# Kernel optimization log

Hardware: AMD Instinct MI355X
Metric: run time of the kernel (lower is better)

The kernel has to match this reference:

```python
import jax, jax.numpy as jnp
import numpy as np

B, S, V, E, Hd, O = 64, 512, 50000, 512, 1024, 10


def setup_inputs() -> dict:
    key = jax.random.key(0)
    ks = jax.random.split(key, 12)
    inp = {
        "inputs": jax.random.randint(ks[0], (B, S), 0, V),
        "weights": jax.random.normal(ks[1], (V, E), dtype=jnp.float32),
        "W_xr": jax.random.normal(ks[2], (E, Hd), dtype=jnp.float32) / np.sqrt(E),
        "W_hr": jax.random.normal(ks[3], (Hd, Hd), dtype=jnp.float32) / np.sqrt(Hd),
        "b_r": jnp.zeros((Hd,), dtype=jnp.float32),
        "W_xz": jax.random.normal(ks[4], (E, Hd), dtype=jnp.float32) / np.sqrt(E),
        "W_hz": jax.random.normal(ks[5], (Hd, Hd), dtype=jnp.float32) / np.sqrt(Hd),
        "b_z": jnp.ones((Hd,), dtype=jnp.float32),
        "W_xc": jax.random.normal(ks[6], (E, Hd), dtype=jnp.float32) / np.sqrt(E),
        "W_hc": jax.random.normal(ks[7], (Hd, Hd), dtype=jnp.float32) / np.sqrt(Hd),
        "b_c": jnp.zeros((Hd,), dtype=jnp.float32),
        "W_hq": jax.random.normal(ks[8], (Hd, O), dtype=jnp.float32) / np.sqrt(Hd),
        "b_q": jnp.zeros((O,), dtype=jnp.float32),
    }
    return inp


def reference(inputs, weights, W_xr, W_hr, b_r, W_xz, W_hz, b_z,
              W_xc, W_hc, b_c, W_hq, b_q):
    # embed: [B, S, E] -> time-major [S, B, E]
    xs = jnp.swapaxes(weights[inputs], 0, 1)

    def step(H, X):
        r = jax.nn.sigmoid(X @ W_xr + H @ W_hr + b_r)
        z = jax.nn.sigmoid(X @ W_xz + H @ W_hz + b_z)
        h = jnp.tanh(X @ W_xc + (H * r) @ W_hc + b_c)
        H_new = z * H + (1.0 - z) * h
        return H_new, None

    H0 = jnp.zeros((inputs.shape[0], W_hr.shape[0]), dtype=weights.dtype)
    H, _ = jax.lax.scan(step, H0, xs)
    return jax.nn.softmax(H @ W_hq + b_q, axis=1)
```

## Files before the change

kernel.cpp:

```cpp
#include <hip/hip_runtime.h>
#include <stdint.h>

#define S_LEN 512
#define B_SZ  64
#define E_DIM 512
#define HD    1024
#define NGATE 3072
#define O_DIM 10

typedef __attribute__((ext_vector_type(4))) float f32x4;
typedef __attribute__((ext_vector_type(8))) short bf16x8;

__device__ __forceinline__ float bf2f(unsigned short u) {
  union { unsigned int i; float f; } c; c.i = ((unsigned int)u) << 16; return c.f;
}
__device__ __forceinline__ unsigned short f2bf(float f) {
  union { float f; unsigned int i; } c; c.f = f;
  unsigned int u = c.i;
  return (unsigned short)((u + 0x7fffu + ((u >> 16) & 1u)) >> 16);
}
__device__ __forceinline__ float sigmoid_fast(float x) { return 1.0f / (1.0f + __expf(-x)); }
__device__ __forceinline__ float tanh_fast(float x) {
  float a = fabsf(x);
  float e = __expf(2.0f * a);
  return copysignf(1.0f - 2.0f / (e + 1.0f), x);
}
__device__ __forceinline__ f32x4 mfma16(bf16x8 a, bf16x8 b, f32x4 c) {
  return __builtin_amdgcn_mfma_f32_16x16x32_bf16(a, b, c, 0, 0, 0);
}
__device__ __forceinline__ unsigned long long ld_u64_agent(const unsigned long long* p) {
  return __hip_atomic_load(p, __ATOMIC_RELAXED, __HIP_MEMORY_SCOPE_AGENT);
}
__device__ __forceinline__ unsigned int ld_u32_agent(const unsigned int* p) {
  return __hip_atomic_load(p, __ATOMIC_RELAXED, __HIP_MEMORY_SCOPE_AGENT);
}
__device__ __forceinline__ void st_u32_agent(unsigned int* p, unsigned int v) {
  __hip_atomic_store(p, v, __ATOMIC_RELAXED, __HIP_MEMORY_SCOPE_AGENT);
}

#define SLOT_STRIDE 64
#define OFF_HB2   0
#define OFF_RH2   262144
#define OFF_HF    393216
#define OFF_SLOTS 655360
#define OFF_WR    1704960
#define OFF_WZ    3802112
#define OFF_WC    5899264
#define OFF_WX    7996416
#define OFF_XP    11142144

__global__ void convert_kernel(const float* __restrict__ Whr, const float* __restrict__ Whz,
                               const float* __restrict__ Whc,
                               const float* __restrict__ Wxr, const float* __restrict__ Wxz,
                               const float* __restrict__ Wxc,
                               unsigned short* __restrict__ Wr_swz, unsigned short* __restrict__ Wz_swz,
                               unsigned short* __restrict__ Wc_swz, unsigned short* __restrict__ Wx_swz) {
  long idx = (long)blockIdx.x * blockDim.x + threadIdx.x;
  const long NH = (long)HD * HD;
  if (idx < 3 * NH) {
    int m = (int)(idx >> 20);
    int t = (int)(idx & (NH - 1));
    int k = t >> 10, j = t & 1023;
    const float* src = (m == 0) ? Whr : (m == 1) ? Whz : Whc;
    unsigned short* dst = (m == 0) ? Wr_swz : (m == 1) ? Wz_swz : Wc_swz;
    int jt = j >> 4, n = j & 15, kt = k >> 5, q = (k >> 3) & 3, i = k & 7;
    dst[((long)(jt * 32 + kt) * 64 + (q * 16 + n)) * 8 + i] = f2bf(src[(long)k * HD + j]);
  } else {
    long t = idx - 3 * NH;
    if (t < (long)E_DIM * NGATE) {
      int e  = (int)(t / NGATE);
      int jg = (int)(t - (long)e * NGATE);
      int jt = jg >> 4, n = jg & 15, kt = e >> 5, q = (e >> 3) & 3, i = e & 7;
      int gate = jg >> 10, jj = jg & 1023;
      const float* src = (gate == 0) ? Wxr : (gate == 1) ? Wxz : Wxc;
      Wx_swz[((long)(jt * 16 + kt) * 64 + (q * 16 + n)) * 8 + i] = f2bf(src[(long)e * HD + jj]);
    }
  }
}

__launch_bounds__(256, 2)
__global__ void embed_kernel(const int* __restrict__ tokens,
                             const float* __restrict__ Emb,
                             const unsigned short* __restrict__ Wx_swz,
                             const float* __restrict__ b_r, const float* __restrict__ b_z,
                             const float* __restrict__ b_c,
                             unsigned short* __restrict__ Xp) {
  __shared__ unsigned short xl[B_SZ * E_DIM];
  const int s = blockIdx.y;
  const int slab = blockIdx.x;
  const int tid = threadIdx.x;
  for (int it = 0; it < 32; ++it) {
    int task = tid + 256 * it;
    int row = task >> 7;
    int f = task & 127;
    int tok = tokens[row * S_LEN + s];
    float4 v = *(const float4*)(Emb + (long)tok * E_DIM + f * 4);
    int sw = (f >> 1) ^ (row & 7);
    unsigned short* p = xl + row * E_DIM + sw * 8 + (f & 1) * 4;
    p[0] = f2bf(v.x); p[1] = f2bf(v.y); p[2] = f2bf(v.z); p[3] = f2bf(v.w);
  }
  __syncthreads();
  const int lane = tid & 63, wave = tid >> 6;
  const int n = lane & 15, q = lane >> 4;
  const int jt_glob = slab * 4 + wave;
  f32x4 acc[4];
  #pragma unroll
  for (int bt = 0; bt < 4; ++bt) { acc[bt][0]=0.f; acc[bt][1]=0.f; acc[bt][2]=0.f; acc[bt][3]=0.f; }
  for (int kt = 0; kt < 16; ++kt) {
    bf16x8 bfrag = *(const bf16x8*)(Wx_swz + ((long)(jt_glob * 16 + kt) * 64 + lane) * 8);
    #pragma unroll
    for (int bt = 0; bt < 4; ++bt) {
      int row = bt * 16 + n;
      int chunk = (kt * 4 + q) ^ (row & 7);
      bf16x8 afrag = *(const bf16x8*)(xl + row * E_DIM + chunk * 8);
      acc[bt] = mfma16(afrag, bfrag, acc[bt]);
    }
  }
  const int jglob = jt_glob * 16 + n;
  const int gate = jglob >> 10, jj = jglob & 1023;
  const float bias = (gate == 0 ? b_r : gate == 1 ? b_z : b_c)[jj];
  #pragma unroll
  for (int bt = 0; bt < 4; ++bt) {
    unsigned int lo = (unsigned)f2bf(acc[bt][0] + bias) | ((unsigned)f2bf(acc[bt][1] + bias) << 16);
    unsigned int hi = (unsigned)f2bf(acc[bt][2] + bias) | ((unsigned)f2bf(acc[bt][3] + bias) << 16);
    uint2 pk; pk.x = lo; pk.y = hi;
    *(uint2*)(Xp + (((long)s * 4 + bt) * NGATE + jglob) * 16 + q * 4) = pk;
  }
}

__launch_bounds__(256, 1)
__global__ void gru_kernel(const unsigned short* __restrict__ Xp,
                           const unsigned short* __restrict__ Wr_swz,
                           const unsigned short* __restrict__ Wz_swz,
                           const unsigned short* __restrict__ Wc_swz,
                           unsigned short* __restrict__ Hb2,
                           float* __restrict__ Hf,
                           unsigned short* __restrict__ rh2,
                           unsigned int* __restrict__ slots) {
  __shared__ float red[4][6][256];
  __shared__ float zbuf[16 * 32];
  __shared__ float hmaster[16 * 32];

  const int tid = threadIdx.x;
  const int lane = tid & 63, w = tid >> 6;
  const int n = lane & 15, q = lane >> 4;
  const int blk = blockIdx.x;
  const int g  = blk & 3;
  const int bh = blk >> 2;

  const int rr = lane >> 4;
  const int m  = lane & 15;
  const int prow = 4 * w + rr;
  const int pc = 2 * m;
  const int t0 = pc >> 4;
  const int n0 = pc & 15;

  bf16x8 wr_reg[2][8], wz_reg[2][8], wc_reg[2][8];
  #pragma unroll
  for (int jt = 0; jt < 2; ++jt)
    #pragma unroll
    for (int t = 0; t < 8; ++t) {
      long o = ((long)((2 * bh + jt) * 32 + w * 8 + t)) * 512 + lane * 8;
      wr_reg[jt][t] = *(const bf16x8*)(Wr_swz + o);
      wz_reg[jt][t] = *(const bf16x8*)(Wz_swz + o);
      wc_reg[jt][t] = *(const bf16x8*)(Wc_swz + o);
    }
  for (int i = tid; i < 512; i += 256) hmaster[i] = 0.f;
  __syncthreads();

  unsigned int* gslots = slots + g * 128 * SLOT_STRIDE;
  unsigned int* myflag = gslots + (bh * 4 + w) * SLOT_STRIDE;
  const unsigned int* pollp =
      gslots + ((w * 8 + (lane >> 2)) * 4 + (lane & 3)) * SLOT_STRIDE;

  const long xp_step = (long)4 * NGATE * 16;
  const unsigned short* xr_p = Xp + ((long)g * NGATE + bh * 32 + pc) * 16 + prow;
  const unsigned short* xc_p = Xp + ((long)g * NGATE + 2 * HD + bh * 32 + pc) * 16 + prow;
  const unsigned short* xz_p = Xp + ((long)g * NGATE + HD + bh * 32 + (w & 1) * 16 + n) * 16 + q * 4;

  unsigned short xr0 = xr_p[0],  xr1 = xr_p[16];
  unsigned short xc0 = xc_p[0],  xc1 = xc_p[16];
  uint2 xz; xz.x = 0; xz.y = 0;
  if (w >= 2) xz = *(const uint2*)xz_p;

  const long my32 = (long)(g * 32 + bh) * 256 + (long)prow * 16 + m;
  const long ld64 = (long)n * 8 + q * 2;
  const long grp64 = (long)g * 4096;

  unsigned int* rh_u32 = (unsigned int*)rh2;
  unsigned int* hb_u32 = (unsigned int*)Hb2;

  unsigned long long a0[8], a1[8];
  #pragma unroll
  for (int t = 0; t < 8; ++t) { a0[t] = 0ull; a1[t] = 0ull; }

  int cur = 0;
  unsigned int seq = 1;

  for (int s = 0; s < S_LEN; ++s) {
    f32x4 aR0, aR1;
    aR0[0]=0.f;aR0[1]=0.f;aR0[2]=0.f;aR0[3]=0.f; aR1 = aR0;
    #pragma unroll
    for (int t = 0; t < 8; ++t) {
      union { unsigned long long u[2]; bf16x8 v; } af;
      af.u[0] = a0[t]; af.u[1] = a1[t];
      aR0 = mfma16(af.v, wr_reg[0][t], aR0);
      aR1 = mfma16(af.v, wr_reg[1][t], aR1);
    }
    *(f32x4*)&red[w][0][lane * 4] = aR0;
    *(f32x4*)&red[w][1][lane * 4] = aR1;
    __syncthreads();
    {
      float v0 = 0.f, v1 = 0.f;
      #pragma unroll
      for (int k = 0; k < 4; ++k) {
        v0 += red[k][t0][(w * 16 + n0) * 4 + rr];
        v1 += red[k][t0][(w * 16 + n0 + 1) * 4 + rr];
      }
      float r0 = sigmoid_fast(v0 + bf2f(xr0)) * hmaster[prow * 32 + pc];
      float r1 = sigmoid_fast(v1 + bf2f(xr1)) * hmaster[prow * 32 + pc + 1];
      unsigned int pay = (unsigned)f2bf(r0) | ((unsigned)f2bf(r1) << 16);
      st_u32_agent(rh_u32 + my32, pay);
      asm volatile("s_waitcnt vmcnt(0)" ::: "memory");
      if (lane == 0) st_u32_agent(myflag, seq);
    }
    f32x4 aZ0, aZ1;
    aZ0[0]=0.f;aZ0[1]=0.f;aZ0[2]=0.f;aZ0[3]=0.f; aZ1 = aZ0;
    #pragma unroll
    for (int t = 0; t < 8; ++t) {
      union { unsigned long long u[2]; bf16x8 v; } af;
      af.u[0] = a0[t]; af.u[1] = a1[t];
      aZ0 = mfma16(af.v, wz_reg[0][t], aZ0);
      aZ1 = mfma16(af.v, wz_reg[1][t], aZ1);
    }
    *(f32x4*)&red[w][2][lane * 4] = aZ0;
    *(f32x4*)&red[w][3][lane * 4] = aZ1;
    if (lane < 32) { while (ld_u32_agent(pollp) < seq) {} }
    asm volatile("" ::: "memory");
    unsigned long long rA[8], rB[8];
    #pragma unroll
    for (int t = 0; t < 8; ++t) {
      const unsigned long long* p =
          (const unsigned long long*)rh2 + grp64 + (long)(w * 8 + t) * 128 + ld64;
      rA[t] = ld_u64_agent(p);
      rB[t] = ld_u64_agent(p + 1);
    }
    __syncthreads();
    if (w >= 2) {
      const int tz = w - 2;
      f32x4 accz = *(const f32x4*)&red[0][2 + tz][lane * 4];
      #pragma unroll
      for (int k = 1; k < 4; ++k) { f32x4 p = *(const f32x4*)&red[k][2 + tz][lane * 4]; accz += p; }
      #pragma unroll
      for (int r_ = 0; r_ < 4; ++r_) {
        float xpv = bf2f((unsigned short)(((r_ < 2) ? xz.x : xz.y) >> ((r_ & 1) * 16)));
        zbuf[(q * 4 + r_) * 32 + tz * 16 + n] = sigmoid_fast(accz[r_] + xpv);
      }
    }
    f32x4 cA, cB;
    cA[0]=0.f;cA[1]=0.f;cA[2]=0.f;cA[3]=0.f; cB = cA;
    #pragma unroll
    for (int t = 0; t < 8; ++t) {
      union { unsigned long long u[2]; bf16x8 v; } af;
      af.u[0] = rA[t]; af.u[1] = rB[t];
      cA = mfma16(af.v, wc_reg[0][t], cA);
      cB = mfma16(af.v, wc_reg[1][t], cB);
    }
    *(f32x4*)&red[w][4][lane * 4] = cA;
    *(f32x4*)&red[w][5][lane * 4] = cB;
    __syncthreads();
    {
      float v0 = 0.f, v1 = 0.f;
      #pragma unroll
      for (int k = 0; k < 4; ++k) {
        v0 += red[k][4 + t0][(w * 16 + n0) * 4 + rr];
        v1 += red[k][4 + t0][(w * 16 + n0 + 1) * 4 + rr];
      }
      float cv0 = tanh_fast(v0 + bf2f(xc0));
      float cv1 = tanh_fast(v1 + bf2f(xc1));
      float z0 = zbuf[prow * 32 + pc],     z1 = zbuf[prow * 32 + pc + 1];
      float h0 = hmaster[prow * 32 + pc],  h1 = hmaster[prow * 32 + pc + 1];
      float hn0 = z0 * h0 + (1.0f - z0) * cv0;
      float hn1 = z1 * h1 + (1.0f - z1) * cv1;
      hmaster[prow * 32 + pc]     = hn0;
      hmaster[prow * 32 + pc + 1] = hn1;
      if (s == S_LEN - 1) {
        Hf[(long)(g * 16 + prow) * HD + bh * 32 + pc]     = hn0;
        Hf[(long)(g * 16 + prow) * HD + bh * 32 + pc + 1] = hn1;
      }
      unsigned int pay = (unsigned)f2bf(hn0) | ((unsigned)f2bf(hn1) << 16);
      st_u32_agent(hb_u32 + (long)(cur ^ 1) * 32768 + my32, pay);
      asm volatile("s_waitcnt vmcnt(0)" ::: "memory");
      if (lane == 0) st_u32_agent(myflag, seq + 1);
    }
    if (s < S_LEN - 1) {
      const unsigned short* xr_s = xr_p + (long)(s + 1) * xp_step;
      const unsigned short* xc_s = xc_p + (long)(s + 1) * xp_step;
      unsigned short xr0n = xr_s[0], xr1n = xr_s[16];
      unsigned short xc0n = xc_s[0], xc1n = xc_s[16];
      uint2 xzn; xzn.x = 0; xzn.y = 0;
      if (w >= 2) xzn = *(const uint2*)(xz_p + (long)(s + 1) * xp_step);
      if (lane < 32) { while (ld_u32_agent(pollp) < seq + 1) {} }
      asm volatile("" ::: "memory");
      const unsigned long long* hb =
          (const unsigned long long*)Hb2 + (long)(cur ^ 1) * 16384 + grp64;
      #pragma unroll
      for (int t = 0; t < 8; ++t) {
        const unsigned long long* p = hb + (long)(w * 8 + t) * 128 + ld64;
        a0[t] = ld_u64_agent(p);
        a1[t] = ld_u64_agent(p + 1);
      }
      xr0 = xr0n; xr1 = xr1n; xc0 = xc0n; xc1 = xc1n; xz = xzn;
    }
    seq += 2;
    cur ^= 1;
  }
}

__global__ void logits_kernel(const float* __restrict__ Hf, const float* __restrict__ Whq,
                              const float* __restrict__ bq, float* __restrict__ out) {
  const int b = blockIdx.x;
  const int lane = threadIdx.x;
  float acc[O_DIM];
  #pragma unroll
  for (int o = 0; o < O_DIM; ++o) acc[o] = 0.f;
  for (int k = lane; k < HD; k += 64) {
    float h = Hf[(long)b * HD + k];
    #pragma unroll
    for (int o = 0; o < O_DIM; ++o) acc[o] += h * Whq[(long)k * O_DIM + o];
  }
  #pragma unroll
  for (int o = 0; o < O_DIM; ++o) {
    #pragma unroll
    for (int off = 32; off > 0; off >>= 1) acc[o] += __shfl_down(acc[o], off, 64);
  }
  if (lane == 0) {
    float lg[O_DIM], m = -1e30f, sum = 0.f;
    #pragma unroll
    for (int o = 0; o < O_DIM; ++o) { lg[o] = acc[o] + bq[o]; m = fmaxf(m, lg[o]); }
    #pragma unroll
    for (int o = 0; o < O_DIM; ++o) { lg[o] = __expf(lg[o] - m); sum += lg[o]; }
    float inv = 1.0f / sum;
    #pragma unroll
    for (int o = 0; o < O_DIM; ++o) out[(long)b * O_DIM + o] = lg[o] * inv;
  }
}

extern "C" void kernel_launch(void* const* d_in, const int* in_sizes, int n_in,
                              void* d_out, int out_size, void* d_ws, size_t ws_size,
                              hipStream_t stream) {
  const int*   tokens = (const int*)d_in[0];
  const float* Emb = (const float*)d_in[1];
  const float* Wxr = (const float*)d_in[2];
  const float* Whr = (const float*)d_in[3];
  const float* br  = (const float*)d_in[4];
  const float* Wxz = (const float*)d_in[5];
  const float* Whz = (const float*)d_in[6];
  const float* bz  = (const float*)d_in[7];
  const float* Wxc = (const float*)d_in[8];
  const float* Whc = (const float*)d_in[9];
  const float* bc  = (const float*)d_in[10];
  const float* Whq = (const float*)d_in[11];
  const float* bq  = (const float*)d_in[12];

  char* ws = (char*)d_ws;
  unsigned short* Hb2    = (unsigned short*)(ws + OFF_HB2);
  unsigned short* rh2    = (unsigned short*)(ws + OFF_RH2);
  float*          Hf     = (float*)(ws + OFF_HF);
  unsigned int*   slots  = (unsigned int*)(ws + OFF_SLOTS);
  unsigned short* Wr_swz = (unsigned short*)(ws + OFF_WR);
  unsigned short* Wz_swz = (unsigned short*)(ws + OFF_WZ);
  unsigned short* Wc_swz = (unsigned short*)(ws + OFF_WC);
  unsigned short* Wx_swz = (unsigned short*)(ws + OFF_WX);
  unsigned short* Xp     = (unsigned short*)(ws + OFF_XP);

  hipMemsetAsync(ws + OFF_SLOTS, 0, 131072, stream);

  convert_kernel<<<18432, 256, 0, stream>>>(Whr, Whz, Whc, Wxr, Wxz, Wxc,
                                            Wr_swz, Wz_swz, Wc_swz, Wx_swz);
  embed_kernel<<<dim3(48, S_LEN), 256, 0, stream>>>(tokens, Emb, Wx_swz, br, bz, bc, Xp);
  gru_kernel<<<128, 256, 0, stream>>>(Xp, Wr_swz, Wz_swz, Wc_swz,
                                      Hb2, Hf, rh2, slots);
  logits_kernel<<<B_SZ, 64, 0, stream>>>(Hf, Whq, bq, (float*)d_out);
}
```

Before: 3.272 ms.

## Replace flag-based barriers with tagged 64-bit payloads for cross-block sync

Each published hidden-state and r*h element now travels as a 64-bit word carrying its step tag in the upper half. Consumers load their data directly and re-poll only entries whose tag is stale, which removes the separate flag write, the store-drain wait and the flag-then-data round trip. The hidden state moves from LDS into registers, and LDS reduction indices are XOR-swizzled with a padded zbuf to cut bank conflicts. In exchange the scratch traffic doubles and the spin loops now re-check 32 values per lane.

```diff
diff --git a/kernel.cpp b/kernel.cpp
--- a/kernel.cpp
+++ b/kernel.cpp
@@ -31,18 +31,16 @@
 __device__ __forceinline__ unsigned long long ld_u64_agent(const unsigned long long* p) {
   return __hip_atomic_load(p, __ATOMIC_RELAXED, __HIP_MEMORY_SCOPE_AGENT);
 }
-__device__ __forceinline__ unsigned int ld_u32_agent(const unsigned int* p) {
-  return __hip_atomic_load(p, __ATOMIC_RELAXED, __HIP_MEMORY_SCOPE_AGENT);
-}
-__device__ __forceinline__ void st_u32_agent(unsigned int* p, unsigned int v) {
+__device__ __forceinline__ void st_u64_agent(unsigned long long* p, unsigned long long v) {
   __hip_atomic_store(p, v, __ATOMIC_RELAXED, __HIP_MEMORY_SCOPE_AGENT);
 }
 
-#define SLOT_STRIDE 64
+__device__ __forceinline__ int ridx(int i) { return i ^ (((i >> 5) & 3) << 3); }
+
 #define OFF_HB2   0
-#define OFF_RH2   262144
-#define OFF_HF    393216
-#define OFF_SLOTS 655360
+#define OFF_RH2   524288
+#define OFF_HF    786432
+#define OFF_ZSCR  786432
 #define OFF_WR    1704960
 #define OFF_WZ    3802112
 #define OFF_WC    5899264
@@ -133,13 +131,11 @@
                            const unsigned short* __restrict__ Wr_swz,
                            const unsigned short* __restrict__ Wz_swz,
                            const unsigned short* __restrict__ Wc_swz,
-                           unsigned short* __restrict__ Hb2,
+                           unsigned long long* __restrict__ Hb2,
                            float* __restrict__ Hf,
-                           unsigned short* __restrict__ rh2,
-                           unsigned int* __restrict__ slots) {
+                           unsigned long long* __restrict__ rh2) {
   __shared__ float red[4][6][256];
-  __shared__ float zbuf[16 * 32];
-  __shared__ float hmaster[16 * 32];
+  __shared__ float zbuf[16 * 33];
 
   const int tid = threadIdx.x;
   const int lane = tid & 63, w = tid >> 6;
@@ -155,6 +151,10 @@
   const int t0 = pc >> 4;
   const int n0 = pc & 15;
 
+  const int sidx  = ridx(lane * 4);
+  const int pidx0 = ridx((w * 16 + n0) * 4 + rr);
+  const int pidx1 = ridx((w * 16 + n0 + 1) * 4 + rr);
+
   bf16x8 wr_reg[2][8], wz_reg[2][8], wc_reg[2][8];
   #pragma unroll
   for (int jt = 0; jt < 2; ++jt)
@@ -165,13 +165,8 @@
       wz_reg[jt][t] = *(const bf16x8*)(Wz_swz + o);
       wc_reg[jt][t] = *(const bf16x8*)(Wc_swz + o);
     }
-  for (int i = tid; i < 512; i += 256) hmaster[i] = 0.f;
-  __syncthreads();
-
-  unsigned int* gslots = slots + g * 128 * SLOT_STRIDE;
-  unsigned int* myflag = gslots + (bh * 4 + w) * SLOT_STRIDE;
-  const unsigned int* pollp =
-      gslots + ((w * 8 + (lane >> 2)) * 4 + (lane & 3)) * SLOT_STRIDE;
+
+  float h0r = 0.f, h1r = 0.f;
 
   const long xp_step = (long)4 * NGATE * 16;
   const unsigned short* xr_p = Xp + ((long)g * NGATE + bh * 32 + pc) * 16 + prow;
@@ -183,115 +178,146 @@
   uint2 xz; xz.x = 0; xz.y = 0;
   if (w >= 2) xz = *(const uint2*)xz_p;
 
-  const long my32 = (long)(g * 32 + bh) * 256 + (long)prow * 16 + m;
-  const long ld64 = (long)n * 8 + q * 2;
-  const long grp64 = (long)g * 4096;
-
-  unsigned int* rh_u32 = (unsigned int*)rh2;
-  unsigned int* hb_u32 = (unsigned int*)Hb2;
-
-  unsigned long long a0[8], a1[8];
-  #pragma unroll
-  for (int t = 0; t < 8; ++t) { a0[t] = 0ull; a1[t] = 0ull; }
+  const long my64 = (long)(g * 32 + bh) * 256 + (long)prow * 16 + m;
+  const long celem = (long)n * 16 + q * 4;
+  const long cbase = (long)(g * 32 + w * 8) * 256 + celem;
+
+  unsigned long long a_[8][4];
+  {
+    const unsigned long long* hb = Hb2 + cbase;
+    #pragma unroll
+    for (int t = 0; t < 8; ++t)
+      #pragma unroll
+      for (int j = 0; j < 4; ++j) a_[t][j] = ld_u64_agent(hb + t * 256 + j);
+  }
 
   int cur = 0;
-  unsigned int seq = 1;
-
   for (int s = 0; s < S_LEN; ++s) {
+    const unsigned int expH = 2u * (unsigned int)s;
+    const unsigned int tagR = expH + 1u;
+    const unsigned int tagH = expH + 2u;
+
+    {
+      const unsigned long long* hb = Hb2 + (long)cur * 32768 + cbase;
+      for (;;) {
+        int nbad = 0;
+        #pragma unroll
+        for (int t = 0; t < 8; ++t)
+          #pragma unroll
+          for (int j = 0; j < 4; ++j)
+            if ((unsigned int)(a_[t][j] >> 32) < expH) {
+              a_[t][j] = ld_u64_agent(hb + t * 256 + j);
+              nbad = 1;
+            }
+        if (!nbad) break;
+      }
+    }
+
     f32x4 aR0, aR1;
     aR0[0]=0.f;aR0[1]=0.f;aR0[2]=0.f;aR0[3]=0.f; aR1 = aR0;
     #pragma unroll
     for (int t = 0; t < 8; ++t) {
-      union { unsigned long long u[2]; bf16x8 v; } af;
-      af.u[0] = a0[t]; af.u[1] = a1[t];
+      union { unsigned int u[4]; bf16x8 v; } af;
+      #pragma unroll
+      for (int j = 0; j < 4; ++j) af.u[j] = (unsigned int)a_[t][j];
       aR0 = mfma16(af.v, wr_reg[0][t], aR0);
       aR1 = mfma16(af.v, wr_reg[1][t], aR1);
     }
-    *(f32x4*)&red[w][0][lane * 4] = aR0;
-    *(f32x4*)&red[w][1][lane * 4] = aR1;
+    *(f32x4*)&red[w][0][sidx] = aR0;
+    *(f32x4*)&red[w][1][sidx] = aR1;
     __syncthreads();
     {
       float v0 = 0.f, v1 = 0.f;
       #pragma unroll
       for (int k = 0; k < 4; ++k) {
-        v0 += red[k][t0][(w * 16 + n0) * 4 + rr];
-        v1 += red[k][t0][(w * 16 + n0 + 1) * 4 + rr];
-      }
-      float r0 = sigmoid_fast(v0 + bf2f(xr0)) * hmaster[prow * 32 + pc];
-      float r1 = sigmoid_fast(v1 + bf2f(xr1)) * hmaster[prow * 32 + pc + 1];
+        v0 += red[k][t0][pidx0];
+        v1 += red[k][t0][pidx1];
+      }
+      float r0 = sigmoid_fast(v0 + bf2f(xr0)) * h0r;
+      float r1 = sigmoid_fast(v1 + bf2f(xr1)) * h1r;
       unsigned int pay = (unsigned)f2bf(r0) | ((unsigned)f2bf(r1) << 16);
-      st_u32_agent(rh_u32 + my32, pay);
-      asm volatile("s_waitcnt vmcnt(0)" ::: "memory");
-      if (lane == 0) st_u32_agent(myflag, seq);
+      st_u64_agent(rh2 + my64, ((unsigned long long)tagR << 32) | pay);
+    }
+    unsigned long long r_[8][4];
+    {
+      const unsigned long long* rb = rh2 + cbase;
+      #pragma unroll
+      for (int t = 0; t < 8; ++t)
+        #pragma unroll
+        for (int j = 0; j < 4; ++j) r_[t][j] = ld_u64_agent(rb + t * 256 + j);
     }
     f32x4 aZ0, aZ1;
     aZ0[0]=0.f;aZ0[1]=0.f;aZ0[2]=0.f;aZ0[3]=0.f; aZ1 = aZ0;
     #pragma unroll
     for (int t = 0; t < 8; ++t) {
-      union { unsigned long long u[2]; bf16x8 v; } af;
-      af.u[0] = a0[t]; af.u[1] = a1[t];
+      union { unsigned int u[4]; bf16x8 v; } af;
+      #pragma unroll
+      for (int j = 0; j < 4; ++j) af.u[j] = (unsigned int)a_[t][j];
       aZ0 = mfma16(af.v, wz_reg[0][t], aZ0);
       aZ1 = mfma16(af.v, wz_reg[1][t], aZ1);
     }
-    *(f32x4*)&red[w][2][lane * 4] = aZ0;
-    *(f32x4*)&red[w][3][lane * 4] = aZ1;
-    if (lane < 32) { while (ld_u32_agent(pollp) < seq) {} }
-    asm volatile("" ::: "memory");
-    unsigned long long rA[8], rB[8];
-    #pragma unroll
-    for (int t = 0; t < 8; ++t) {
-      const unsigned long long* p =
-          (const unsigned long long*)rh2 + grp64 + (long)(w * 8 + t) * 128 + ld64;
-      rA[t] = ld_u64_agent(p);
-      rB[t] = ld_u64_agent(p + 1);
+    *(f32x4*)&red[w][2][sidx] = aZ0;
+    *(f32x4*)&red[w][3][sidx] = aZ1;
+    {
+      const unsigned long long* rb = rh2 + cbase;
+      for (;;) {
+        int nbad = 0;
+        #pragma unroll
+        for (int t = 0; t < 8; ++t)
+          #pragma unroll
+          for (int j = 0; j < 4; ++j)
+            if ((unsigned int)(r_[t][j] >> 32) < tagR) {
+              r_[t][j] = ld_u64_agent(rb + t * 256 + j);
+              nbad = 1;
+            }
+        if (!nbad) break;
+      }
     }
     __syncthreads();
     if (w >= 2) {
       const int tz = w - 2;
-      f32x4 accz = *(const f32x4*)&red[0][2 + tz][lane * 4];
-      #pragma unroll
-      for (int k = 1; k < 4; ++k) { f32x4 p = *(const f32x4*)&red[k][2 + tz][lane * 4]; accz += p; }
-      #pragma unroll
-      for (int r_ = 0; r_ < 4; ++r_) {
-        float xpv = bf2f((unsigned short)(((r_ < 2) ? xz.x : xz.y) >> ((r_ & 1) * 16)));
-        zbuf[(q * 4 + r_) * 32 + tz * 16 + n] = sigmoid_fast(accz[r_] + xpv);
+      f32x4 accz = *(const f32x4*)&red[0][2 + tz][sidx];
+      #pragma unroll
+      for (int k = 1; k < 4; ++k) { f32x4 p = *(const f32x4*)&red[k][2 + tz][sidx]; accz += p; }
+      #pragma unroll
+      for (int r_i = 0; r_i < 4; ++r_i) {
+        float xpv = bf2f((unsigned short)(((r_i < 2) ? xz.x : xz.y) >> ((r_i & 1) * 16)));
+        zbuf[(q * 4 + r_i) * 33 + tz * 16 + n] = sigmoid_fast(accz[r_i] + xpv);
       }
     }
     f32x4 cA, cB;
     cA[0]=0.f;cA[1]=0.f;cA[2]=0.f;cA[3]=0.f; cB = cA;
     #pragma unroll
     for (int t = 0; t < 8; ++t) {
-      union { unsigned long long u[2]; bf16x8 v; } af;
-      af.u[0] = rA[t]; af.u[1] = rB[t];
+      union { unsigned int u[4]; bf16x8 v; } af;
+      #pragma unroll
+      for (int j = 0; j < 4; ++j) af.u[j] = (unsigned int)r_[t][j];
       cA = mfma16(af.v, wc_reg[0][t], cA);
       cB = mfma16(af.v, wc_reg[1][t], cB);
     }
-    *(f32x4*)&red[w][4][lane * 4] = cA;
-    *(f32x4*)&red[w][5][lane * 4] = cB;
+    *(f32x4*)&red[w][4][sidx] = cA;
+    *(f32x4*)&red[w][5][sidx] = cB;
     __syncthreads();
     {
       float v0 = 0.f, v1 = 0.f;
       #pragma unroll
       for (int k = 0; k < 4; ++k) {
-        v0 += red[k][4 + t0][(w * 16 + n0) * 4 + rr];
-        v1 += red[k][4 + t0][(w * 16 + n0 + 1) * 4 + rr];
+        v0 += red[k][4 + t0][pidx0];
+        v1 += red[k][4 + t0][pidx1];
       }
       float cv0 = tanh_fast(v0 + bf2f(xc0));
       float cv1 = tanh_fast(v1 + bf2f(xc1));
-      float z0 = zbuf[prow * 32 + pc],     z1 = zbuf[prow * 32 + pc + 1];
-      float h0 = hmaster[prow * 32 + pc],  h1 = hmaster[prow * 32 + pc + 1];
-      float hn0 = z0 * h0 + (1.0f - z0) * cv0;
-      float hn1 = z1 * h1 + (1.0f - z1) * cv1;
-      hmaster[prow * 32 + pc]     = hn0;
-      hmaster[prow * 32 + pc + 1] = hn1;
+      float z0 = zbuf[prow * 33 + pc], z1 = zbuf[prow * 33 + pc + 1];
+      float hn0 = z0 * h0r + (1.0f - z0) * cv0;
+      float hn1 = z1 * h1r + (1.0f - z1) * cv1;
+      h0r = hn0; h1r = hn1;
       if (s == S_LEN - 1) {
         Hf[(long)(g * 16 + prow) * HD + bh * 32 + pc]     = hn0;
         Hf[(long)(g * 16 + prow) * HD + bh * 32 + pc + 1] = hn1;
       }
       unsigned int pay = (unsigned)f2bf(hn0) | ((unsigned)f2bf(hn1) << 16);
-      st_u32_agent(hb_u32 + (long)(cur ^ 1) * 32768 + my32, pay);
-      asm volatile("s_waitcnt vmcnt(0)" ::: "memory");
-      if (lane == 0) st_u32_agent(myflag, seq + 1);
+      st_u64_agent(Hb2 + (long)(cur ^ 1) * 32768 + my64,
+                   ((unsigned long long)tagH << 32) | pay);
     }
     if (s < S_LEN - 1) {
       const unsigned short* xr_s = xr_p + (long)(s + 1) * xp_step;
@@ -300,19 +326,13 @@
       unsigned short xc0n = xc_s[0], xc1n = xc_s[16];
       uint2 xzn; xzn.x = 0; xzn.y = 0;
       if (w >= 2) xzn = *(const uint2*)(xz_p + (long)(s + 1) * xp_step);
-      if (lane < 32) { while (ld_u32_agent(pollp) < seq + 1) {} }
-      asm volatile("" ::: "memory");
-      const unsigned long long* hb =
-          (const unsigned long long*)Hb2 + (long)(cur ^ 1) * 16384 + grp64;
-      #pragma unroll
-      for (int t = 0; t < 8; ++t) {
-        const unsigned long long* p = hb + (long)(w * 8 + t) * 128 + ld64;
-        a0[t] = ld_u64_agent(p);
-        a1[t] = ld_u64_agent(p + 1);
-      }
+      const unsigned long long* hb = Hb2 + (long)(cur ^ 1) * 32768 + cbase;
+      #pragma unroll
+      for (int t = 0; t < 8; ++t)
+        #pragma unroll
+        for (int j = 0; j < 4; ++j) a_[t][j] = ld_u64_agent(hb + t * 256 + j);
       xr0 = xr0n; xr1 = xr1n; xc0 = xc0n; xc1 = xc1n; xz = xzn;
     }
-    seq += 2;
     cur ^= 1;
   }
 }
@@ -364,22 +384,20 @@
   const float* bq  = (const float*)d_in[12];
 
   char* ws = (char*)d_ws;
-  unsigned short* Hb2    = (unsigned short*)(ws + OFF_HB2);
-  unsigned short* rh2    = (unsigned short*)(ws + OFF_RH2);
+  unsigned long long* Hb2 = (unsigned long long*)(ws + OFF_HB2);
+  unsigned long long* rh2 = (unsigned long long*)(ws + OFF_RH2);
   float*          Hf     = (float*)(ws + OFF_HF);
-  unsigned int*   slots  = (unsigned int*)(ws + OFF_SLOTS);
   unsigned short* Wr_swz = (unsigned short*)(ws + OFF_WR);
   unsigned short* Wz_swz = (unsigned short*)(ws + OFF_WZ);
   unsigned short* Wc_swz = (unsigned short*)(ws + OFF_WC);
   unsigned short* Wx_swz = (unsigned short*)(ws + OFF_WX);
   unsigned short* Xp     = (unsigned short*)(ws + OFF_XP);
 
-  hipMemsetAsync(ws + OFF_SLOTS, 0, 131072, stream);
+  hipMemsetAsync(ws, 0, OFF_ZSCR, stream);
 
   convert_kernel<<<18432, 256, 0, stream>>>(Whr, Whz, Whc, Wxr, Wxz, Wxc,
                                             Wr_swz, Wz_swz, Wc_swz, Wx_swz);
   embed_kernel<<<dim3(48, S_LEN), 256, 0, stream>>>(tokens, Emb, Wx_swz, br, bz, bc, Xp);
-  gru_kernel<<<128, 256, 0, stream>>>(Xp, Wr_swz, Wz_swz, Wc_swz,
-                                      Hb2, Hf, rh2, slots);
+  gru_kernel<<<128, 256, 0, stream>>>(Xp, Wr_swz, Wz_swz, Wc_swz, Hb2, Hf, rh2);
   logits_kernel<<<B_SZ, 64, 0, stream>>>(Hf, Whq, bq, (float*)d_out);
 }
```

Result: slower. 6.980 ms (+113.3%).

## Swizzle LDS reduction buffers, keep hidden state in registers, defer flag store

Applied to the files above, without the earlier changes.

XOR-swizzles the shared reduction buffer indices and pads zbuf to cut LDS bank conflicts in the cross-wave reductions. The per-thread hidden state moves from shared memory into registers, which drops the hmaster buffer and its initial barrier. The wait on the r*h store and the flag publish are moved to after the z-gate MFMAs, so the store latency overlaps useful compute. The risk is that the swizzled write and read indices must stay consistent, and that delaying the flag lets peer blocks start later.

```diff
diff --git a/kernel.cpp b/kernel.cpp
--- a/kernel.cpp
+++ b/kernel.cpp
@@ -37,6 +37,8 @@
 __device__ __forceinline__ void st_u32_agent(unsigned int* p, unsigned int v) {
   __hip_atomic_store(p, v, __ATOMIC_RELAXED, __HIP_MEMORY_SCOPE_AGENT);
 }
+
+__device__ __forceinline__ int swz(int i) { return i ^ (((i >> 5) & 7) << 2); }
 
 #define SLOT_STRIDE 64
 #define OFF_HB2   0
@@ -138,8 +140,7 @@
                            unsigned short* __restrict__ rh2,
                            unsigned int* __restrict__ slots) {
   __shared__ float red[4][6][256];
-  __shared__ float zbuf[16 * 32];
-  __shared__ float hmaster[16 * 32];
+  __shared__ float zbuf[16 * 33];
 
   const int tid = threadIdx.x;
   const int lane = tid & 63, w = tid >> 6;
@@ -155,6 +156,10 @@
   const int t0 = pc >> 4;
   const int n0 = pc & 15;
 
+  const int sidx  = swz(lane * 4);
+  const int pidx0 = swz((w * 16 + n0) * 4 + rr);
+  const int pidx1 = swz((w * 16 + n0 + 1) * 4 + rr);
+
   bf16x8 wr_reg[2][8], wz_reg[2][8], wc_reg[2][8];
   #pragma unroll
   for (int jt = 0; jt < 2; ++jt)
@@ -165,8 +170,8 @@
       wz_reg[jt][t] = *(const bf16x8*)(Wz_swz + o);
       wc_reg[jt][t] = *(const bf16x8*)(Wc_swz + o);
     }
-  for (int i = tid; i < 512; i += 256) hmaster[i] = 0.f;
-  __syncthreads();
+
+  float h0r = 0.f, h1r = 0.f;
 
   unsigned int* gslots = slots + g * 128 * SLOT_STRIDE;
   unsigned int* myflag = gslots + (bh * 4 + w) * SLOT_STRIDE;
@@ -207,22 +212,20 @@
       aR0 = mfma16(af.v, wr_reg[0][t], aR0);
       aR1 = mfma16(af.v, wr_reg[1][t], aR1);
     }
-    *(f32x4*)&red[w][0][lane * 4] = aR0;
-    *(f32x4*)&red[w][1][lane * 4] = aR1;
+    *(f32x4*)&red[w][0][sidx] = aR0;
+    *(f32x4*)&red[w][1][sidx] = aR1;
     __syncthreads();
     {
       float v0 = 0.f, v1 = 0.f;
       #pragma unroll
       for (int k = 0; k < 4; ++k) {
-        v0 += red[k][t0][(w * 16 + n0) * 4 + rr];
-        v1 += red[k][t0][(w * 16 + n0 + 1) * 4 + rr];
-      }
-      float r0 = sigmoid_fast(v0 + bf2f(xr0)) * hmaster[prow * 32 + pc];
-      float r1 = sigmoid_fast(v1 + bf2f(xr1)) * hmaster[prow * 32 + pc + 1];
+        v0 += red[k][t0][pidx0];
+        v1 += red[k][t0][pidx1];
+      }
+      float r0 = sigmoid_fast(v0 + bf2f(xr0)) * h0r;
+      float r1 = sigmoid_fast(v1 + bf2f(xr1)) * h1r;
       unsigned int pay = (unsigned)f2bf(r0) | ((unsigned)f2bf(r1) << 16);
       st_u32_agent(rh_u32 + my32, pay);
-      asm volatile("s_waitcnt vmcnt(0)" ::: "memory");
-      if (lane == 0) st_u32_agent(myflag, seq);
     }
     f32x4 aZ0, aZ1;
     aZ0[0]=0.f;aZ0[1]=0.f;aZ0[2]=0.f;aZ0[3]=0.f; aZ1 = aZ0;
@@ -233,8 +236,10 @@
       aZ0 = mfma16(af.v, wz_reg[0][t], aZ0);
       aZ1 = mfma16(af.v, wz_reg[1][t], aZ1);
     }
-    *(f32x4*)&red[w][2][lane * 4] = aZ0;
-    *(f32x4*)&red[w][3][lane * 4] = aZ1;
+    *(f32x4*)&red[w][2][sidx] = aZ0;
+    *(f32x4*)&red[w][3][sidx] = aZ1;
+    asm volatile("s_waitcnt vmcnt(0)" ::: "memory");
+    if (lane == 0) st_u32_agent(myflag, seq);
     if (lane < 32) { while (ld_u32_agent(pollp) < seq) {} }
     asm volatile("" ::: "memory");
     unsigned long long rA[8], rB[8];
@@ -248,13 +253,13 @@
     __syncthreads();
     if (w >= 2) {
       const int tz = w - 2;
-      f32x4 accz = *(const f32x4*)&red[0][2 + tz][lane * 4];
-      #pragma unroll
-      for (int k = 1; k < 4; ++k) { f32x4 p = *(const f32x4*)&red[k][2 + tz][lane * 4]; accz += p; }
+      f32x4 accz = *(const f32x4*)&red[0][2 + tz][sidx];
+      #pragma unroll
+      for (int k = 1; k < 4; ++k) { f32x4 p = *(const f32x4*)&red[k][2 + tz][sidx]; accz += p; }
       #pragma unroll
       for (int r_ = 0; r_ < 4; ++r_) {
         float xpv = bf2f((unsigned short)(((r_ < 2) ? xz.x : xz.y) >> ((r_ & 1) * 16)));
-        zbuf[(q * 4 + r_) * 32 + tz * 16 + n] = sigmoid_fast(accz[r_] + xpv);
+        zbuf[(q * 4 + r_) * 33 + tz * 16 + n] = sigmoid_fast(accz[r_] + xpv);
       }
     }
     f32x4 cA, cB;
@@ -266,24 +271,22 @@
       cA = mfma16(af.v, wc_reg[0][t], cA);
       cB = mfma16(af.v, wc_reg[1][t], cB);
     }
-    *(f32x4*)&red[w][4][lane * 4] = cA;
-    *(f32x4*)&red[w][5][lane * 4] = cB;
+    *(f32x4*)&red[w][4][sidx] = cA;
+    *(f32x4*)&red[w][5][sidx] = cB;
     __syncthreads();
     {
       float v0 = 0.f, v1 = 0.f;
       #pragma unroll
       for (int k = 0; k < 4; ++k) {
-        v0 += red[k][4 + t0][(w * 16 + n0) * 4 + rr];
-        v1 += red[k][4 + t0][(w * 16 + n0 + 1) * 4 + rr];
+        v0 += red[k][4 + t0][pidx0];
+        v1 += red[k][4 + t0][pidx1];
       }
       float cv0 = tanh_fast(v0 + bf2f(xc0));
       float cv1 = tanh_fast(v1 + bf2f(xc1));
-      float z0 = zbuf[prow * 32 + pc],     z1 = zbuf[prow * 32 + pc + 1];
-      float h0 = hmaster[prow * 32 + pc],  h1 = hmaster[prow * 32 + pc + 1];
-      float hn0 = z0 * h0 + (1.0f - z0) * cv0;
-      float hn1 = z1 * h1 + (1.0f - z1) * cv1;
-      hmaster[prow * 32 + pc]     = hn0;
-      hmaster[prow * 32 + pc + 1] = hn1;
+      float z0 = zbuf[prow * 33 + pc], z1 = zbuf[prow * 33 + pc + 1];
+      float hn0 = z0 * h0r + (1.0f - z0) * cv0;
+      float hn1 = z1 * h1r + (1.0f - z1) * cv1;
+      h0r = hn0; h1r = hn1;
       if (s == S_LEN - 1) {
         Hf[(long)(g * 16 + prow) * HD + bh * 32 + pc]     = hn0;
         Hf[(long)(g * 16 + prow) * HD + bh * 32 + pc + 1] = hn1;
```

Result: slower. 3.410 ms (+4.2%).
